# Optimization experiments

Measured on AMD Instinct MI355X. Metric: run time of the kernel, lower is better.

## Reference

```python
import jax, jax.numpy as jnp
import numpy as np

IGNORE_LABEL = 255
EPS = 1e-12  # F.normalize eps


def _l2norm(x, axis):
    n = jnp.sqrt(jnp.sum(x * x, axis=axis, keepdims=True))
    return x / jnp.maximum(n, EPS)


def setup_inputs() -> dict:
    key = jax.random.key(0)
    k1, k2, k3, k4, k5 = jax.random.split(key, 5)
    B, H, W, A, C = 4, 128, 128, 1024, 6
    N = B * H * W
    return {
        "Proto": jax.random.normal(k1, (C, A), dtype=jnp.float32),
        "srcfeat": jax.random.normal(k2, (N, A), dtype=jnp.float32),
        "tarfeat": jax.random.normal(k3, (B, A, H, W), dtype=jnp.float32),
        "tarout": jax.random.normal(k4, (B, C, H, W), dtype=jnp.float32),
        "labels": jax.random.randint(k5, (N,), 0, C, dtype=jnp.int64),
    }


def reference(Proto, srcfeat, tarfeat, tarout, labels):
    C, A = Proto.shape

    # ---- per-class mean of srcfeat (exact replacement of onehot expand+mul+sum) ----
    mask = labels != IGNORE_LABEL                           # (N,)
    feats = srcfeat * mask[:, None].astype(srcfeat.dtype)   # zero out ignored pixels
    seg = jnp.where(mask, labels, C)                        # route ignored pixels to dump segment C
    sums = jax.ops.segment_sum(feats, seg, num_segments=C + 1)[:C]            # (C, A)
    counts = jax.ops.segment_sum(mask.astype(srcfeat.dtype), seg, num_segments=C + 1)[:C]  # (C,)
    mean = sums / jnp.maximum(counts, 1.0)[:, None]          # (C, A)

    # ---- contrast_cal: cosine similarity of target features against prototypes ----
    n, c, h, w = tarfeat.shape
    Xn = _l2norm(tarfeat, axis=1)                            # normalize over channel dim
    X_ = Xn.transpose(0, 2, 3, 1).reshape(-1, c)             # (n*h*w, c)
    Yn = _l2norm(Proto.reshape(C, A), axis=-1)               # (C, A)
    contrast = (X_ @ Yn.T).reshape(n, h, w, C).transpose(0, 3, 1, 2)  # (n, C, h, w)

    # ---- forward_loss: softmax over class dim ----
    a1 = jax.nn.softmax(tarout, axis=1)
    b = 1.0 - contrast
    loss1 = jnp.mean(jnp.sum(a1 * b, axis=1))

    # ---- reverse_loss: softmax over flattened pixel dim per class ----
    a2 = jax.nn.softmax(tarout.transpose(1, 0, 2, 3).reshape(C, -1), axis=1)  # (C, n*h*w)
    b2 = b.transpose(1, 0, 2, 3).reshape(C, -1)
    loss2 = jnp.mean(jnp.sum(a2 * b2, axis=1))

    return (loss1 + loss2, mean)
```

## Files before the change

kernel.cpp:

```cpp
#include <hip/hip_runtime.h>
#include <hip/hip_bf16.h>
#include <math.h>

#define A_DIM 1024
#define C_DIM 6
#define N_PIX 65536
#define HW 16384
#define S1_BLOCKS 512
#define S1_ROWS 128

#define WS_ACC  0
#define WS_YN   64
#define WS_P1   (WS_YN + C_DIM * A_DIM)
#define WS_P2   (WS_P1 + S1_BLOCKS * C_DIM * A_DIM)

__global__ void k_zero(float* __restrict__ acc) {
    if (threadIdx.x < 64) acc[threadIdx.x] = 0.0f;
}

__global__ __launch_bounds__(256) void k_src_stage1(
        const float* __restrict__ src, const int* __restrict__ labels,
        float* __restrict__ part, float* __restrict__ counts) {
    const int t = threadIdx.x;
    const int g = blockIdx.x;
    const int row0 = g * S1_ROWS;

    float acc[C_DIM][4];
#pragma unroll
    for (int c = 0; c < C_DIM; ++c)
#pragma unroll
        for (int j = 0; j < 4; ++j) acc[c][j] = 0.0f;
    int cnt[C_DIM] = {0, 0, 0, 0, 0, 0};

#pragma unroll 2
    for (int r = 0; r < S1_ROWS; ++r) {
        const int row = row0 + r;
        const int lab = labels[row];
        const float* p = src + (size_t)row * A_DIM + t;
        float x0 = p[0];
        float x1 = p[256];
        float x2 = p[512];
        float x3 = p[768];
#pragma unroll
        for (int c = 0; c < C_DIM; ++c) {
            float m = (lab == c) ? 1.0f : 0.0f;
            acc[c][0] = fmaf(m, x0, acc[c][0]);
            acc[c][1] = fmaf(m, x1, acc[c][1]);
            acc[c][2] = fmaf(m, x2, acc[c][2]);
            acc[c][3] = fmaf(m, x3, acc[c][3]);
        }
        if (t == 0) {
#pragma unroll
            for (int c = 0; c < C_DIM; ++c) cnt[c] += (lab == c) ? 1 : 0;
        }
    }

    float* dst = part + (size_t)g * (C_DIM * A_DIM);
#pragma unroll
    for (int c = 0; c < C_DIM; ++c)
#pragma unroll
        for (int j = 0; j < 4; ++j)
            dst[c * A_DIM + j * 256 + t] = acc[c][j];

    if (t == 0) {
#pragma unroll
        for (int c = 0; c < C_DIM; ++c) atomicAdd(&counts[c], (float)cnt[c]);
    }
}

__global__ __launch_bounds__(256) void k_src_stage2a(
        const float* __restrict__ part, float* __restrict__ part2) {
    const int tid = blockIdx.x * 256 + threadIdx.x;
    const int j = tid % (C_DIM * A_DIM);
    const int chunk = tid / (C_DIM * A_DIM);
    const float* p = part + (size_t)chunk * 32 * (C_DIM * A_DIM) + j;
    float s = 0.0f;
#pragma unroll 4
    for (int i = 0; i < 32; ++i) s += p[(size_t)i * (C_DIM * A_DIM)];
    part2[tid] = s;
}

__global__ __launch_bounds__(256) void k_src_stage2b(
        const float* __restrict__ part2, const float* __restrict__ counts,
        float* __restrict__ out_mean) {
    const int j = blockIdx.x * 256 + threadIdx.x;
    float s = 0.0f;
#pragma unroll
    for (int i = 0; i < 16; ++i) s += part2[i * (C_DIM * A_DIM) + j];
    const int c = j >> 10;
    out_mean[j] = s / fmaxf(counts[c], 1.0f);
}

__global__ __launch_bounds__(256) void k_proto_norm(
        const float* __restrict__ proto, float* __restrict__ yn) {
    const int c = blockIdx.x;
    const int t = threadIdx.x;
    const float* row = proto + c * A_DIM;
    float ss = 0.0f;
#pragma unroll
    for (int j = 0; j < 4; ++j) {
        float x = row[t + j * 256];
        ss = fmaf(x, x, ss);
    }
    for (int off = 32; off > 0; off >>= 1) ss += __shfl_down(ss, off, 64);
    __shared__ float sred[4];
    if ((t & 63) == 0) sred[t >> 6] = ss;
    __syncthreads();
    const float tot = sred[0] + sred[1] + sred[2] + sred[3];
    const float inv = 1.0f / fmaxf(sqrtf(tot), 1e-12f);
#pragma unroll
    for (int j = 0; j < 4; ++j) yn[c * A_DIM + t + j * 256] = row[t + j * 256] * inv;
}

__global__ __launch_bounds__(256) void k_zsum(
        const float* __restrict__ tarout, float* __restrict__ Z) {
    const int c = blockIdx.x >> 4;
    const int chunk = blockIdx.x & 15;
    const int q0 = chunk * 4096;
    const int t = threadIdx.x;
    const int b = q0 >> 14;
    const int hw0 = q0 & (HW - 1);
    const float* p = tarout + ((size_t)(b * C_DIM + c) << 14) + hw0;
    float s = 0.0f;
#pragma unroll
    for (int i = 0; i < 16; ++i) s += __expf(p[i * 256 + t]);
    for (int off = 32; off > 0; off >>= 1) s += __shfl_down(s, off, 64);
    __shared__ float sred[4];
    if ((t & 63) == 0) sred[t >> 6] = s;
    __syncthreads();
    if (t == 0) atomicAdd(&Z[c], sred[0] + sred[1] + sred[2] + sred[3]);
}

__global__ __launch_bounds__(256) void k_main(
        const float* __restrict__ tarfeat, const float* __restrict__ tarout,
        const float* __restrict__ yn, const float* __restrict__ Z,
        float* __restrict__ lossacc) {
    __shared__ __align__(16) float s_yn[C_DIM * A_DIM];
    __shared__ float red[7][4][64];

    const int t = threadIdx.x;
#pragma unroll
    for (int i = 0; i < 24; ++i) s_yn[i * 256 + t] = yn[i * 256 + t];
    __syncthreads();

    const int wave = t >> 6;
    const int lane = t & 63;
    const int p = blockIdx.x * 64 + lane;
    const int b = p >> 14;
    const int hw = p & (HW - 1);
    const float* xp = tarfeat + ((size_t)b << 24) + hw;
    const int a0 = wave * 256;

    float ns = 0.0f;
    float d0 = 0.0f, d1 = 0.0f, d2 = 0.0f, d3 = 0.0f, d4 = 0.0f, d5 = 0.0f;
    for (int k = 0; k < 64; ++k) {
        const int a = a0 + k * 4;
        float x0 = xp[(size_t)(a + 0) << 14];
        float x1 = xp[(size_t)(a + 1) << 14];
        float x2 = xp[(size_t)(a + 2) << 14];
        float x3 = xp[(size_t)(a + 3) << 14];
        float4 y0 = *(const float4*)(s_yn + 0 * A_DIM + a);
        float4 y1 = *(const float4*)(s_yn + 1 * A_DIM + a);
        float4 y2 = *(const float4*)(s_yn + 2 * A_DIM + a);
        float4 y3 = *(const float4*)(s_yn + 3 * A_DIM + a);
        float4 y4 = *(const float4*)(s_yn + 4 * A_DIM + a);
        float4 y5 = *(const float4*)(s_yn + 5 * A_DIM + a);
        ns = fmaf(x0, x0, ns); ns = fmaf(x1, x1, ns);
        ns = fmaf(x2, x2, ns); ns = fmaf(x3, x3, ns);
        d0 = fmaf(x0, y0.x, d0); d0 = fmaf(x1, y0.y, d0); d0 = fmaf(x2, y0.z, d0); d0 = fmaf(x3, y0.w, d0);
        d1 = fmaf(x0, y1.x, d1); d1 = fmaf(x1, y1.y, d1); d1 = fmaf(x2, y1.z, d1); d1 = fmaf(x3, y1.w, d1);
        d2 = fmaf(x0, y2.x, d2); d2 = fmaf(x1, y2.y, d2); d2 = fmaf(x2, y2.z, d2); d2 = fmaf(x3, y2.w, d2);
        d3 = fmaf(x0, y3.x, d3); d3 = fmaf(x1, y3.y, d3); d3 = fmaf(x2, y3.z, d3); d3 = fmaf(x3, y3.w, d3);
        d4 = fmaf(x0, y4.x, d4); d4 = fmaf(x1, y4.y, d4); d4 = fmaf(x2, y4.z, d4); d4 = fmaf(x3, y4.w, d4);
        d5 = fmaf(x0, y5.x, d5); d5 = fmaf(x1, y5.y, d5); d5 = fmaf(x2, y5.z, d5); d5 = fmaf(x3, y5.w, d5);
    }

    red[0][wave][lane] = ns;
    red[1][wave][lane] = d0;
    red[2][wave][lane] = d1;
    red[3][wave][lane] = d2;
    red[4][wave][lane] = d3;
    red[5][wave][lane] = d4;
    red[6][wave][lane] = d5;
    __syncthreads();

    if (t < 64) {
        float v[7];
#pragma unroll
        for (int i = 0; i < 7; ++i)
            v[i] = red[i][0][t] + red[i][1][t] + red[i][2][t] + red[i][3][t];
        const float inv = 1.0f / fmaxf(sqrtf(v[0]), 1e-12f);

        const int p2 = blockIdx.x * 64 + t;
        const int bb = p2 >> 14;
        const int hw2 = p2 & (HW - 1);
        float tv[6];
#pragma unroll
        for (int c = 0; c < C_DIM; ++c)
            tv[c] = tarout[((size_t)(bb * C_DIM + c) << 14) + hw2];

        float m = tv[0];
#pragma unroll
        for (int c = 1; c < C_DIM; ++c) m = fmaxf(m, tv[c]);
        float ex[6], ssum = 0.0f;
#pragma unroll
        for (int c = 0; c < C_DIM; ++c) { ex[c] = __expf(tv[c] - m); ssum += ex[c]; }

        float l1p = 0.0f, l2p = 0.0f;
#pragma unroll
        for (int c = 0; c < C_DIM; ++c) {
            const float bc = 1.0f - v[1 + c] * inv;
            l1p = fmaf(ex[c], bc, l1p);
            l2p = fmaf(__expf(tv[c]) * (1.0f / Z[c]), bc, l2p);
        }
        float l1 = l1p / ssum;
        float l2 = l2p;
        for (int off = 32; off > 0; off >>= 1) {
            l1 += __shfl_down(l1, off, 64);
            l2 += __shfl_down(l2, off, 64);
        }
        if (t == 0) {
            atomicAdd(lossacc + 0, l1);
            atomicAdd(lossacc + 1, l2);
        }
    }
}

__global__ void k_final(const float* __restrict__ acc, float* __restrict__ out) {
    if (threadIdx.x == 0)
        out[0] = acc[6] / (float)N_PIX + acc[7] / (float)C_DIM;
}

extern "C" void kernel_launch(void* const* d_in, const int* in_sizes, int n_in,
                              void* d_out, int out_size, void* d_ws, size_t ws_size,
                              hipStream_t stream) {
    const float* Proto   = (const float*)d_in[0];
    const float* srcfeat = (const float*)d_in[1];
    const float* tarfeat = (const float*)d_in[2];
    const float* tarout  = (const float*)d_in[3];
    const int*   labels  = (const int*)d_in[4];
    float* out = (float*)d_out;

    float* w     = (float*)d_ws;
    float* accs  = w + WS_ACC;
    float* yn    = w + WS_YN;
    float* part1 = w + WS_P1;
    float* part2 = w + WS_P2;

    k_zero<<<1, 64, 0, stream>>>(accs);
    k_proto_norm<<<C_DIM, 256, 0, stream>>>(Proto, yn);
    k_zsum<<<C_DIM * 16, 256, 0, stream>>>(tarout, accs);
    k_src_stage1<<<S1_BLOCKS, 256, 0, stream>>>(srcfeat, labels, part1, accs + 8);
    k_src_stage2a<<<384, 256, 0, stream>>>(part1, part2);
    k_src_stage2b<<<24, 256, 0, stream>>>(part2, accs + 8, out + 1);
    k_main<<<N_PIX / 64, 256, 0, stream>>>(tarfeat, tarout, yn, accs, accs + 6);
    k_final<<<1, 64, 0, stream>>>(accs, out);
}
```

Before: 586.2 us.

## Fold softmax denominator into main kernel and merge init launches

The separate Z-sum pass over tarout is removed. The reverse-loss softmax denominator and numerator are now accumulated per class inside the main kernel, and their ratio is taken in the final kernel. Zeroing and prototype normalization are merged into one launch. The source stage-1 kernel now stages labels in shared memory, uses float4 loads and stores, and counts labels once at the end. This cuts launches and one read of tarout, but adds 12 extra wave shuffles per reduction step and 12 atomics per block, and uses unshifted exponentials that could overflow for large logits.

```diff
diff --git a/kernel.cpp b/kernel.cpp
--- a/kernel.cpp
+++ b/kernel.cpp
@@ -14,8 +14,30 @@
 #define WS_P1   (WS_YN + C_DIM * A_DIM)
 #define WS_P2   (WS_P1 + S1_BLOCKS * C_DIM * A_DIM)
 
-__global__ void k_zero(float* __restrict__ acc) {
-    if (threadIdx.x < 64) acc[threadIdx.x] = 0.0f;
+__global__ __launch_bounds__(256) void k_init(
+        const float* __restrict__ proto, float* __restrict__ yn,
+        float* __restrict__ accs) {
+    const int t = threadIdx.x;
+    if (blockIdx.x == C_DIM) {
+        if (t < 64) accs[t] = 0.0f;
+        return;
+    }
+    const int c = blockIdx.x;
+    const float* row = proto + c * A_DIM;
+    float ss = 0.0f;
+#pragma unroll
+    for (int j = 0; j < 4; ++j) {
+        float x = row[t + j * 256];
+        ss = fmaf(x, x, ss);
+    }
+    for (int off = 32; off > 0; off >>= 1) ss += __shfl_down(ss, off, 64);
+    __shared__ float sred[4];
+    if ((t & 63) == 0) sred[t >> 6] = ss;
+    __syncthreads();
+    const float tot = sred[0] + sred[1] + sred[2] + sred[3];
+    const float inv = 1.0f / fmaxf(sqrtf(tot), 1e-12f);
+#pragma unroll
+    for (int j = 0; j < 4; ++j) yn[c * A_DIM + t + j * 256] = row[t + j * 256] * inv;
 }
 
 __global__ __launch_bounds__(256) void k_src_stage1(
@@ -25,44 +47,42 @@
     const int g = blockIdx.x;
     const int row0 = g * S1_ROWS;
 
+    __shared__ int slab[S1_ROWS];
+    if (t < S1_ROWS) slab[t] = labels[row0 + t];
+    __syncthreads();
+
     float acc[C_DIM][4];
 #pragma unroll
     for (int c = 0; c < C_DIM; ++c)
 #pragma unroll
         for (int j = 0; j < 4; ++j) acc[c][j] = 0.0f;
-    int cnt[C_DIM] = {0, 0, 0, 0, 0, 0};
-
+
+    const float4* sp = (const float4*)src + (size_t)row0 * 256 + t;
 #pragma unroll 2
     for (int r = 0; r < S1_ROWS; ++r) {
-        const int row = row0 + r;
-        const int lab = labels[row];
-        const float* p = src + (size_t)row * A_DIM + t;
-        float x0 = p[0];
-        float x1 = p[256];
-        float x2 = p[512];
-        float x3 = p[768];
+        const int lab = slab[r];
+        const float4 x = sp[(size_t)r * 256];
 #pragma unroll
         for (int c = 0; c < C_DIM; ++c) {
-            float m = (lab == c) ? 1.0f : 0.0f;
-            acc[c][0] = fmaf(m, x0, acc[c][0]);
-            acc[c][1] = fmaf(m, x1, acc[c][1]);
-            acc[c][2] = fmaf(m, x2, acc[c][2]);
-            acc[c][3] = fmaf(m, x3, acc[c][3]);
-        }
-        if (t == 0) {
-#pragma unroll
-            for (int c = 0; c < C_DIM; ++c) cnt[c] += (lab == c) ? 1 : 0;
-        }
-    }
-
-    float* dst = part + (size_t)g * (C_DIM * A_DIM);
+            const float m = (lab == c) ? 1.0f : 0.0f;
+            acc[c][0] = fmaf(m, x.x, acc[c][0]);
+            acc[c][1] = fmaf(m, x.y, acc[c][1]);
+            acc[c][2] = fmaf(m, x.z, acc[c][2]);
+            acc[c][3] = fmaf(m, x.w, acc[c][3]);
+        }
+    }
+
+    float4* dst = (float4*)(part + (size_t)g * (C_DIM * A_DIM)) + t;
 #pragma unroll
     for (int c = 0; c < C_DIM; ++c)
-#pragma unroll
-        for (int j = 0; j < 4; ++j)
-            dst[c * A_DIM + j * 256 + t] = acc[c][j];
+        dst[c * 256] = make_float4(acc[c][0], acc[c][1], acc[c][2], acc[c][3]);
 
     if (t == 0) {
+        int cnt[C_DIM] = {0, 0, 0, 0, 0, 0};
+        for (int r = 0; r < S1_ROWS; ++r) {
+            const int lab = slab[r];
+            if ((unsigned)lab < C_DIM) ++cnt[lab];
+        }
 #pragma unroll
         for (int c = 0; c < C_DIM; ++c) atomicAdd(&counts[c], (float)cnt[c]);
     }
@@ -91,50 +111,9 @@
     out_mean[j] = s / fmaxf(counts[c], 1.0f);
 }
 
-__global__ __launch_bounds__(256) void k_proto_norm(
-        const float* __restrict__ proto, float* __restrict__ yn) {
-    const int c = blockIdx.x;
-    const int t = threadIdx.x;
-    const float* row = proto + c * A_DIM;
-    float ss = 0.0f;
-#pragma unroll
-    for (int j = 0; j < 4; ++j) {
-        float x = row[t + j * 256];
-        ss = fmaf(x, x, ss);
-    }
-    for (int off = 32; off > 0; off >>= 1) ss += __shfl_down(ss, off, 64);
-    __shared__ float sred[4];
-    if ((t & 63) == 0) sred[t >> 6] = ss;
-    __syncthreads();
-    const float tot = sred[0] + sred[1] + sred[2] + sred[3];
-    const float inv = 1.0f / fmaxf(sqrtf(tot), 1e-12f);
-#pragma unroll
-    for (int j = 0; j < 4; ++j) yn[c * A_DIM + t + j * 256] = row[t + j * 256] * inv;
-}
-
-__global__ __launch_bounds__(256) void k_zsum(
-        const float* __restrict__ tarout, float* __restrict__ Z) {
-    const int c = blockIdx.x >> 4;
-    const int chunk = blockIdx.x & 15;
-    const int q0 = chunk * 4096;
-    const int t = threadIdx.x;
-    const int b = q0 >> 14;
-    const int hw0 = q0 & (HW - 1);
-    const float* p = tarout + ((size_t)(b * C_DIM + c) << 14) + hw0;
-    float s = 0.0f;
-#pragma unroll
-    for (int i = 0; i < 16; ++i) s += __expf(p[i * 256 + t]);
-    for (int off = 32; off > 0; off >>= 1) s += __shfl_down(s, off, 64);
-    __shared__ float sred[4];
-    if ((t & 63) == 0) sred[t >> 6] = s;
-    __syncthreads();
-    if (t == 0) atomicAdd(&Z[c], sred[0] + sred[1] + sred[2] + sred[3]);
-}
-
 __global__ __launch_bounds__(256) void k_main(
         const float* __restrict__ tarfeat, const float* __restrict__ tarout,
-        const float* __restrict__ yn, const float* __restrict__ Z,
-        float* __restrict__ lossacc) {
+        const float* __restrict__ yn, float* __restrict__ accs) {
     __shared__ __align__(16) float s_yn[C_DIM * A_DIM];
     __shared__ float red[7][4][64];
 
@@ -153,6 +132,7 @@
 
     float ns = 0.0f;
     float d0 = 0.0f, d1 = 0.0f, d2 = 0.0f, d3 = 0.0f, d4 = 0.0f, d5 = 0.0f;
+#pragma unroll 2
     for (int k = 0; k < 64; ++k) {
         const int a = a0 + k * 4;
         float x0 = xp[(size_t)(a + 0) << 14];
@@ -194,7 +174,7 @@
         const int p2 = blockIdx.x * 64 + t;
         const int bb = p2 >> 14;
         const int hw2 = p2 & (HW - 1);
-        float tv[6];
+        float tv[C_DIM];
 #pragma unroll
         for (int c = 0; c < C_DIM; ++c)
             tv[c] = tarout[((size_t)(bb * C_DIM + c) << 14) + hw2];
@@ -202,33 +182,48 @@
         float m = tv[0];
 #pragma unroll
         for (int c = 1; c < C_DIM; ++c) m = fmaxf(m, tv[c]);
-        float ex[6], ssum = 0.0f;
+        const float em = __expf(m);
+        float ex[C_DIM], ssum = 0.0f;
 #pragma unroll
         for (int c = 0; c < C_DIM; ++c) { ex[c] = __expf(tv[c] - m); ssum += ex[c]; }
 
-        float l1p = 0.0f, l2p = 0.0f;
+        float l1p = 0.0f;
+        float zp[C_DIM], np[C_DIM];
 #pragma unroll
         for (int c = 0; c < C_DIM; ++c) {
             const float bc = 1.0f - v[1 + c] * inv;
             l1p = fmaf(ex[c], bc, l1p);
-            l2p = fmaf(__expf(tv[c]) * (1.0f / Z[c]), bc, l2p);
+            const float eraw = ex[c] * em;
+            zp[c] = eraw;
+            np[c] = eraw * bc;
         }
         float l1 = l1p / ssum;
-        float l2 = l2p;
         for (int off = 32; off > 0; off >>= 1) {
             l1 += __shfl_down(l1, off, 64);
-            l2 += __shfl_down(l2, off, 64);
+#pragma unroll
+            for (int c = 0; c < C_DIM; ++c) {
+                zp[c] += __shfl_down(zp[c], off, 64);
+                np[c] += __shfl_down(np[c], off, 64);
+            }
         }
         if (t == 0) {
-            atomicAdd(lossacc + 0, l1);
-            atomicAdd(lossacc + 1, l2);
+            atomicAdd(accs + 6, l1);
+#pragma unroll
+            for (int c = 0; c < C_DIM; ++c) {
+                atomicAdd(accs + c, zp[c]);
+                atomicAdd(accs + 16 + c, np[c]);
+            }
         }
     }
 }
 
 __global__ void k_final(const float* __restrict__ acc, float* __restrict__ out) {
-    if (threadIdx.x == 0)
-        out[0] = acc[6] / (float)N_PIX + acc[7] / (float)C_DIM;
+    if (threadIdx.x == 0) {
+        float l2 = 0.0f;
+#pragma unroll
+        for (int c = 0; c < C_DIM; ++c) l2 += acc[16 + c] / acc[c];
+        out[0] = acc[6] / (float)N_PIX + l2 / (float)C_DIM;
+    }
 }
 
 extern "C" void kernel_launch(void* const* d_in, const int* in_sizes, int n_in,
@@ -247,12 +242,10 @@
     float* part1 = w + WS_P1;
     float* part2 = w + WS_P2;
 
-    k_zero<<<1, 64, 0, stream>>>(accs);
-    k_proto_norm<<<C_DIM, 256, 0, stream>>>(Proto, yn);
-    k_zsum<<<C_DIM * 16, 256, 0, stream>>>(tarout, accs);
+    k_init<<<C_DIM + 1, 256, 0, stream>>>(Proto, yn, accs);
     k_src_stage1<<<S1_BLOCKS, 256, 0, stream>>>(srcfeat, labels, part1, accs + 8);
     k_src_stage2a<<<384, 256, 0, stream>>>(part1, part2);
     k_src_stage2b<<<24, 256, 0, stream>>>(part2, accs + 8, out + 1);
-    k_main<<<N_PIX / 64, 256, 0, stream>>>(tarfeat, tarout, yn, accs, accs + 6);
+    k_main<<<N_PIX / 64, 256, 0, stream>>>(tarfeat, tarout, yn, accs);
     k_final<<<1, 64, 0, stream>>>(accs, out);
 }
```

Result: slower. 648.4 us (+10.6%).
